# Kernel optimization log

Measured on AMD Instinct MI355X. Metric: run time of the kernel, lower is better.

## Reference

```python
import jax, jax.numpy as jnp
import numpy as np

EMBED_DIM = 1024
NUM_HEADS = 16
HEAD_DIM = EMBED_DIM // NUM_HEADS


def setup_inputs() -> dict:
    key = jax.random.key(0)
    ks = jax.random.split(key, 9)
    s = 1.0 / np.sqrt(EMBED_DIM)
    mk = lambda k: jax.random.uniform(k, (EMBED_DIM, EMBED_DIM), jnp.float32, -s, s)
    bk = lambda k: jax.random.uniform(k, (EMBED_DIM,), jnp.float32, -s, s)
    return {
        "input_tensor": jax.random.normal(ks[0], (4, 2048, EMBED_DIM), jnp.float32),
        "wq": mk(ks[1]), "bq": bk(ks[2]),
        "wk": mk(ks[3]), "bk_": bk(ks[4]),
        "wv": mk(ks[5]), "bv": bk(ks[6]),
        "wo": mk(ks[7]), "bo": bk(ks[8]),
    }


def reference(input_tensor, wq, bq, wk, bk_, wv, bv, wo, bo):
    B, S, E = input_tensor.shape
    H, D = NUM_HEADS, HEAD_DIM
    # torch Linear: y = x @ W.T + b
    q = input_tensor @ wq.T + bq
    k = input_tensor @ wk.T + bk_
    v = input_tensor @ wv.T + bv
    q = q.reshape(B, S, H, D).transpose(0, 2, 1, 3)  # [B,H,S,D]
    k = k.reshape(B, S, H, D).transpose(0, 2, 1, 3)
    v = v.reshape(B, S, H, D).transpose(0, 2, 1, 3)
    scores = jnp.einsum('bhsd,bhtd->bhst', q, k) / jnp.sqrt(jnp.float32(D))
    attn = jax.nn.softmax(scores, axis=-1)  # dropout p=0 -> identity
    out = jnp.einsum('bhst,bhtd->bhsd', attn, v)
    out = out.transpose(0, 2, 1, 3).reshape(B, S, E)
    return out @ wo.T + bo
```

## Files before the change

### kernel.cpp

```cpp
#include <hip/hip_runtime.h>

typedef __bf16 bf16x8 __attribute__((ext_vector_type(8)));
typedef float  f32x4  __attribute__((ext_vector_type(4)));
typedef float  f32x16 __attribute__((ext_vector_type(16)));
typedef unsigned u32x4 __attribute__((ext_vector_type(4)));

#define NB 4
#define SEQ 2048
#define EMB 1024
#define NH 16
#define HD 64
#define MTOT (NB * SEQ)

__device__ __forceinline__ unsigned short f2bf(float f) {
    unsigned u = __float_as_uint(f);
    return (unsigned short)((u + 0x7fffu + ((u >> 16) & 1u)) >> 16);
}

__device__ __forceinline__ void gload16(const void* g, void* l) {
    __builtin_amdgcn_global_load_lds(
        (const __attribute__((address_space(1))) unsigned int*)g,
        (__attribute__((address_space(3))) unsigned int*)l,
        16, 0, 0);
}

__global__ __launch_bounds__(256) void cast_f32_bf16(
    const float* __restrict__ src, unsigned short* __restrict__ dst, int n4) {
    int i = blockIdx.x * 256 + threadIdx.x;
    if (i < n4) {
        float4 v = ((const float4*)src)[i];
        ushort4 r;
        r.x = f2bf(v.x); r.y = f2bf(v.y); r.z = f2bf(v.z); r.w = f2bf(v.w);
        ((ushort4*)dst)[i] = r;
    }
}

__global__ __launch_bounds__(256) void cast4_f32_bf16(
    const float* __restrict__ a, const float* __restrict__ b,
    const float* __restrict__ c, const float* __restrict__ d,
    unsigned short* __restrict__ oa, unsigned short* __restrict__ ob,
    unsigned short* __restrict__ oc, unsigned short* __restrict__ od) {
    int which = blockIdx.x >> 10;
    int i = (blockIdx.x & 1023) * 256 + threadIdx.x;
    const float* src = which == 0 ? a : which == 1 ? b : which == 2 ? c : d;
    unsigned short* dst = which == 0 ? oa : which == 1 ? ob : which == 2 ? oc : od;
    float4 v = ((const float4*)src)[i];
    ushort4 r;
    r.x = f2bf(v.x); r.y = f2bf(v.y); r.z = f2bf(v.z); r.w = f2bf(v.w);
    ((ushort4*)dst)[i] = r;
}

__global__ __launch_bounds__(256) void gemm_qkv(
    const unsigned short* __restrict__ A, const unsigned short* __restrict__ W3,
    const float* __restrict__ bq, const float* __restrict__ bk,
    const float* __restrict__ bv, unsigned short* __restrict__ Qo,
    unsigned short* __restrict__ Ko, unsigned short* __restrict__ Vto) {
    constexpr int K = EMB;
    __shared__ __align__(16) unsigned short As[128 * 64];
    __shared__ __align__(16) unsigned short Bs[128 * 64];

    const int lane = threadIdx.x & 63;
    const int wv   = threadIdx.x >> 6;
    const int wr   = wv >> 1, wc = wv & 1;
    const int m0   = blockIdx.y * 128, n0 = blockIdx.x * 128;
    const int proj = n0 >> 10;
    const float* bp = proj == 0 ? bq : proj == 1 ? bk : bv;
    const float oscale = proj == 0 ? 0.18033688011112043f : 1.0f;

    f32x4 acc[4][4];
#pragma unroll
    for (int a = 0; a < 4; ++a)
#pragma unroll
        for (int b = 0; b < 4; ++b) acc[a][b] = (f32x4){0.f, 0.f, 0.f, 0.f};

    const int gsw = ((lane & 7) ^ (lane >> 3)) * 8;
    for (int kt = 0; kt < K / 64; ++kt) {
        if (kt) __syncthreads();
#pragma unroll
        for (int j = 0; j < 4; ++j) {
            int rb = (wv * 4 + j) * 8;
            int r  = rb + (lane >> 3);
            gload16(A + (size_t)(m0 + r) * K + kt * 64 + gsw, &As[rb * 64]);
            gload16(W3 + (size_t)(n0 + r) * K + kt * 64 + gsw, &Bs[rb * 64]);
        }
        __syncthreads();
#pragma unroll
        for (int ks = 0; ks < 2; ++ks) {
            const int slot = ((ks * 4 + (lane >> 4)) ^ (lane & 7)) * 8;
            bf16x8 af[4], bf_[4];
#pragma unroll
            for (int x = 0; x < 4; ++x) {
                af[x]  = *(const bf16x8*)&As[(wr * 64 + x * 16 + (lane & 15)) * 64 + slot];
                bf_[x] = *(const bf16x8*)&Bs[(wc * 64 + x * 16 + (lane & 15)) * 64 + slot];
            }
#pragma unroll
            for (int mi = 0; mi < 4; ++mi)
#pragma unroll
                for (int ni = 0; ni < 4; ++ni)
                    acc[mi][ni] = __builtin_amdgcn_mfma_f32_16x16x32_bf16(
                        af[mi], bf_[ni], acc[mi][ni], 0, 0, 0);
        }
    }

#pragma unroll
    for (int mi = 0; mi < 4; ++mi) {
#pragma unroll
        for (int ni = 0; ni < 4; ++ni) {
            int n    = n0 + wc * 64 + ni * 16 + (lane & 15);
            int nloc = n & 1023;
            float bvv = bp[nloc];
            int h = nloc >> 6, d = nloc & 63;
#pragma unroll
            for (int i = 0; i < 4; ++i) {
                int m = m0 + wr * 64 + mi * 16 + (lane >> 4) * 4 + i;
                float v = (acc[mi][ni][i] + bvv) * oscale;
                int b = m >> 11, s = m & (SEQ - 1);
                if (proj == 0)
                    Qo[(((size_t)(b * NH + h) * SEQ + s) << 6) + d] = f2bf(v);
                else if (proj == 1)
                    Ko[(((size_t)(b * NH + h) * SEQ + s) << 6) + d] = f2bf(v);
                else
                    Vto[((size_t)(b * NH + h) * 64 + d) * SEQ + s] = f2bf(v);
            }
        }
    }
}

__global__ __launch_bounds__(256) void gemm_out(
    const unsigned short* __restrict__ A, const unsigned short* __restrict__ W,
    const float* __restrict__ bias, float* __restrict__ out) {
    constexpr int K = EMB;
    __shared__ __align__(16) unsigned short As[128 * 64];
    __shared__ __align__(16) unsigned short Bs[128 * 64];

    const int lane = threadIdx.x & 63;
    const int wv   = threadIdx.x >> 6;
    const int wr   = wv >> 1, wc = wv & 1;
    const int m0   = blockIdx.y * 128, n0 = blockIdx.x * 128;

    f32x4 acc[4][4];
#pragma unroll
    for (int a = 0; a < 4; ++a)
#pragma unroll
        for (int b = 0; b < 4; ++b) acc[a][b] = (f32x4){0.f, 0.f, 0.f, 0.f};

    const int gsw = ((lane & 7) ^ (lane >> 3)) * 8;
    for (int kt = 0; kt < K / 64; ++kt) {
        if (kt) __syncthreads();
#pragma unroll
        for (int j = 0; j < 4; ++j) {
            int rb = (wv * 4 + j) * 8;
            int r  = rb + (lane >> 3);
            gload16(A + (size_t)(m0 + r) * K + kt * 64 + gsw, &As[rb * 64]);
            gload16(W + (size_t)(n0 + r) * K + kt * 64 + gsw, &Bs[rb * 64]);
        }
        __syncthreads();
#pragma unroll
        for (int ks = 0; ks < 2; ++ks) {
            const int slot = ((ks * 4 + (lane >> 4)) ^ (lane & 7)) * 8;
            bf16x8 af[4], bf_[4];
#pragma unroll
            for (int x = 0; x < 4; ++x) {
                af[x]  = *(const bf16x8*)&As[(wr * 64 + x * 16 + (lane & 15)) * 64 + slot];
                bf_[x] = *(const bf16x8*)&Bs[(wc * 64 + x * 16 + (lane & 15)) * 64 + slot];
            }
#pragma unroll
            for (int mi = 0; mi < 4; ++mi)
#pragma unroll
                for (int ni = 0; ni < 4; ++ni)
                    acc[mi][ni] = __builtin_amdgcn_mfma_f32_16x16x32_bf16(
                        af[mi], bf_[ni], acc[mi][ni], 0, 0, 0);
        }
    }

#pragma unroll
    for (int mi = 0; mi < 4; ++mi) {
#pragma unroll
        for (int ni = 0; ni < 4; ++ni) {
            int n = n0 + wc * 64 + ni * 16 + (lane & 15);
            float bv = bias[n];
#pragma unroll
            for (int i = 0; i < 4; ++i) {
                int m = m0 + wr * 64 + mi * 16 + (lane >> 4) * 4 + i;
                out[(size_t)m * EMB + n] = acc[mi][ni][i] + bv;
            }
        }
    }
}

__global__ __launch_bounds__(512, 4) void attn_fwd(
    const unsigned short* __restrict__ Q, const unsigned short* __restrict__ K,
    const unsigned short* __restrict__ Vt, unsigned short* __restrict__ AO) {
    const int qt = blockIdx.x;
    const int bh = blockIdx.y;
    const int lane = threadIdx.x & 63;
    const int wv   = threadIdx.x >> 6;
    const int l31  = lane & 31;
    const int lh   = lane >> 5;

    __shared__ __align__(16) unsigned short Ks[2][64 * 64];
    __shared__ __align__(16) unsigned short Vs[2][64 * 64];

    const unsigned short* Kb = K + (size_t)bh * SEQ * HD;
    const unsigned short* Vb = Vt + (size_t)bh * HD * SEQ;

    const unsigned short* Qp = Q + ((size_t)bh * SEQ + qt * 256 + wv * 32 + l31) * HD + lh * 8;
    bf16x8 qfr[4];
#pragma unroll
    for (int kc = 0; kc < 4; ++kc) qfr[kc] = *(const bf16x8*)(Qp + kc * 16);

    f32x16 oT[2];
#pragma unroll
    for (int r = 0; r < 16; ++r) { oT[0][r] = 0.f; oT[1][r] = 0.f; }
    float lacc = 0.f;

    auto stageKV = [&](int buf, int t) {
        int r  = wv * 8 + (lane >> 3);
        int gs = (lane & 7) ^ (r & 7);
        gload16(Kb + (size_t)(t * 64 + r) * 64 + gs * 8, &Ks[buf][wv * 8 * 64]);
        gload16(Vb + (size_t)r * SEQ + t * 64 + gs * 8, &Vs[buf][wv * 8 * 64]);
    };

    stageKV(0, 0);

    for (int t = 0; t < SEQ / 64; ++t) {
        const int cur = t & 1;
        __syncthreads();
        if (t + 1 < SEQ / 64) stageKV(cur ^ 1, t + 1);

#pragma unroll
        for (int sub = 0; sub < 2; ++sub) {
            f32x16 st;
#pragma unroll
            for (int r = 0; r < 16; ++r) st[r] = 0.f;
            const int krow = sub * 32 + l31;
            __builtin_amdgcn_s_setprio(1);
#pragma unroll
            for (int kc = 0; kc < 4; ++kc) {
                int slot = (kc * 2 + lh) ^ (krow & 7);
                bf16x8 kf = *(const bf16x8*)&Ks[cur][krow * 64 + slot * 8];
                st = __builtin_amdgcn_mfma_f32_32x32x16_bf16(kf, qfr[kc], st, 0, 0, 0);
            }
            __builtin_amdgcn_s_setprio(0);

            unsigned w0, w1, w2, w3, w4, w5, w6, w7;
#define EXPPK(WI, RA, RB)                                                     \
            {                                                                 \
                float pa = __builtin_amdgcn_exp2f(st[RA]);                    \
                float pb = __builtin_amdgcn_exp2f(st[RB]);                    \
                lacc += pa + pb;                                              \
                asm("v_cvt_pk_bf16_f32 %0, %1, %2" : "=v"(WI) : "v"(pa), "v"(pb)); \
            }
            EXPPK(w0, 0, 1)  EXPPK(w1, 2, 3)  EXPPK(w2, 4, 5)  EXPPK(w3, 6, 7)
            EXPPK(w4, 8, 9)  EXPPK(w5, 10, 11) EXPPK(w6, 12, 13) EXPPK(w7, 14, 15)
#undef EXPPK
            asm volatile("v_permlane32_swap_b32 %0, %1" : "+v"(w0), "+v"(w2));
            asm volatile("v_permlane32_swap_b32 %0, %1" : "+v"(w1), "+v"(w3));
            asm volatile("v_permlane32_swap_b32 %0, %1" : "+v"(w4), "+v"(w6));
            asm volatile("v_permlane32_swap_b32 %0, %1" : "+v"(w5), "+v"(w7));
            u32x4 a0 = {w0, w1, w2, w3};
            u32x4 a1 = {w4, w5, w6, w7};
            bf16x8 pf0 = __builtin_bit_cast(bf16x8, a0);
            bf16x8 pf1 = __builtin_bit_cast(bf16x8, a1);

            __builtin_amdgcn_s_setprio(1);
#pragma unroll
            for (int dt = 0; dt < 2; ++dt) {
                int d = dt * 32 + l31;
#pragma unroll
                for (int ks = 0; ks < 2; ++ks) {
                    int slot = (sub * 4 + ks * 2 + lh) ^ (d & 7);
                    bf16x8 vf = *(const bf16x8*)&Vs[cur][d * 64 + slot * 8];
                    oT[dt] = __builtin_amdgcn_mfma_f32_32x32x16_bf16(
                        vf, ks ? pf1 : pf0, oT[dt], 0, 0, 0);
                }
            }
            __builtin_amdgcn_s_setprio(0);
        }
    }

    float l = lacc + __shfl_xor(lacc, 32);
    float inv = 1.0f / l;
    const int b = bh >> 4, h = bh & 15;
    const int q = qt * 256 + wv * 32 + l31;
    unsigned short* aor = AO + (((size_t)b * SEQ + q) * NH + h) * HD;
#pragma unroll
    for (int dt = 0; dt < 2; ++dt) {
#pragma unroll
        for (int g = 0; g < 4; ++g) {
            ushort4 o;
            o.x = f2bf(oT[dt][g * 4 + 0] * inv);
            o.y = f2bf(oT[dt][g * 4 + 1] * inv);
            o.z = f2bf(oT[dt][g * 4 + 2] * inv);
            o.w = f2bf(oT[dt][g * 4 + 3] * inv);
            *(ushort4*)(aor + dt * 32 + g * 8 + lh * 4) = o;
        }
    }
}

extern "C" void kernel_launch(void* const* d_in, const int* in_sizes, int n_in,
                              void* d_out, int out_size, void* d_ws, size_t ws_size,
                              hipStream_t stream) {
    const float* X  = (const float*)d_in[0];
    const float* wq = (const float*)d_in[1];
    const float* bq = (const float*)d_in[2];
    const float* wk = (const float*)d_in[3];
    const float* bk = (const float*)d_in[4];
    const float* wv = (const float*)d_in[5];
    const float* bv = (const float*)d_in[6];
    const float* wo = (const float*)d_in[7];
    const float* bo = (const float*)d_in[8];
    float* out = (float*)d_out;

    unsigned short* ws = (unsigned short*)d_ws;
    const size_t XE = (size_t)MTOT * EMB;
    const size_t WE = (size_t)EMB * EMB;
    unsigned short* Xb  = ws;
    unsigned short* Wqb = ws + XE;
    unsigned short* Wkb = Wqb + WE;
    unsigned short* Wvb = Wkb + WE;
    unsigned short* Wob = Wvb + WE;
    unsigned short* Qb  = Wob + WE;
    unsigned short* Kb  = Qb + XE;
    unsigned short* Vtb = Kb + XE;
    unsigned short* AOb = Xb;

    cast_f32_bf16<<<(int)(XE / 4 / 256), 256, 0, stream>>>(X, Xb, (int)(XE / 4));
    cast4_f32_bf16<<<4096, 256, 0, stream>>>(wq, wk, wv, wo, Wqb, Wkb, Wvb, Wob);

    gemm_qkv<<<dim3(3 * EMB / 128, MTOT / 128), 256, 0, stream>>>(
        Xb, Wqb, bq, bk, bv, Qb, Kb, Vtb);

    attn_fwd<<<dim3(SEQ / 256, NB * NH), 512, 0, stream>>>(Qb, Kb, Vtb, AOb);

    gemm_out<<<dim3(EMB / 128, MTOT / 128), 256, 0, stream>>>(AOb, Wob, bo, out);
}
```

Before: 189.9 us.

## Process two 32-row query groups per wave to reuse K/V fragments in attention

Each wave in the attention kernel now owns 64 query rows split into two 32-row groups. The K fragments loaded from LDS are reused for both score MFMAs, and the V fragments for both PV MFMAs, halving LDS reads per unit of MFMA work. Blocks shrink to 4 waves, each wave staging two rows of K/V, and the grid becomes 1D with bh as the fast index so blocks sharing a head's K/V run close together. Register pressure roughly doubles for accumulators and Q fragments, and the launch bounds change to 256 threads with 2 blocks per SIMD, which may lower occupancy.

```diff
diff --git a/kernel.cpp b/kernel.cpp
--- a/kernel.cpp
+++ b/kernel.cpp
@@ -188,11 +188,11 @@
     }
 }
 
-__global__ __launch_bounds__(512, 4) void attn_fwd(
+__global__ __launch_bounds__(256, 2) void attn_fwd(
     const unsigned short* __restrict__ Q, const unsigned short* __restrict__ K,
     const unsigned short* __restrict__ Vt, unsigned short* __restrict__ AO) {
-    const int qt = blockIdx.x;
-    const int bh = blockIdx.y;
+    const int qt = blockIdx.x >> 6;
+    const int bh = blockIdx.x & 63;
     const int lane = threadIdx.x & 63;
     const int wv   = threadIdx.x >> 6;
     const int l31  = lane & 31;
@@ -204,21 +204,33 @@
     const unsigned short* Kb = K + (size_t)bh * SEQ * HD;
     const unsigned short* Vb = Vt + (size_t)bh * HD * SEQ;
 
-    const unsigned short* Qp = Q + ((size_t)bh * SEQ + qt * 256 + wv * 32 + l31) * HD + lh * 8;
-    bf16x8 qfr[4];
-#pragma unroll
-    for (int kc = 0; kc < 4; ++kc) qfr[kc] = *(const bf16x8*)(Qp + kc * 16);
-
-    f32x16 oT[2];
-#pragma unroll
-    for (int r = 0; r < 16; ++r) { oT[0][r] = 0.f; oT[1][r] = 0.f; }
-    float lacc = 0.f;
+    bf16x8 qfr[2][4];
+#pragma unroll
+    for (int qg = 0; qg < 2; ++qg) {
+        const unsigned short* Qp =
+            Q + ((size_t)bh * SEQ + qt * 256 + wv * 64 + qg * 32 + l31) * HD + lh * 8;
+#pragma unroll
+        for (int kc = 0; kc < 4; ++kc) qfr[qg][kc] = *(const bf16x8*)(Qp + kc * 16);
+    }
+
+    f32x16 oT[2][2];
+#pragma unroll
+    for (int qg = 0; qg < 2; ++qg)
+#pragma unroll
+        for (int dt = 0; dt < 2; ++dt)
+#pragma unroll
+            for (int r = 0; r < 16; ++r) oT[qg][dt][r] = 0.f;
+    float lacc[2] = {0.f, 0.f};
 
     auto stageKV = [&](int buf, int t) {
-        int r  = wv * 8 + (lane >> 3);
-        int gs = (lane & 7) ^ (r & 7);
-        gload16(Kb + (size_t)(t * 64 + r) * 64 + gs * 8, &Ks[buf][wv * 8 * 64]);
-        gload16(Vb + (size_t)r * SEQ + t * 64 + gs * 8, &Vs[buf][wv * 8 * 64]);
+#pragma unroll
+        for (int j = 0; j < 2; ++j) {
+            int rb = wv * 16 + j * 8;
+            int r  = rb + (lane >> 3);
+            int gs = (lane & 7) ^ (r & 7);
+            gload16(Kb + (size_t)(t * 64 + r) * 64 + gs * 8, &Ks[buf][rb * 64]);
+            gload16(Vb + (size_t)r * SEQ + t * 64 + gs * 8, &Vs[buf][rb * 64]);
+        }
     };
 
     stageKV(0, 0);
@@ -230,38 +242,52 @@
 
 #pragma unroll
         for (int sub = 0; sub < 2; ++sub) {
-            f32x16 st;
-#pragma unroll
-            for (int r = 0; r < 16; ++r) st[r] = 0.f;
             const int krow = sub * 32 + l31;
-            __builtin_amdgcn_s_setprio(1);
+            bf16x8 kf[4];
 #pragma unroll
             for (int kc = 0; kc < 4; ++kc) {
                 int slot = (kc * 2 + lh) ^ (krow & 7);
-                bf16x8 kf = *(const bf16x8*)&Ks[cur][krow * 64 + slot * 8];
-                st = __builtin_amdgcn_mfma_f32_32x32x16_bf16(kf, qfr[kc], st, 0, 0, 0);
-            }
+                kf[kc] = *(const bf16x8*)&Ks[cur][krow * 64 + slot * 8];
+            }
+            f32x16 stA, stB;
+#pragma unroll
+            for (int r = 0; r < 16; ++r) { stA[r] = 0.f; stB[r] = 0.f; }
+            __builtin_amdgcn_s_setprio(1);
+#pragma unroll
+            for (int kc = 0; kc < 4; ++kc)
+                stA = __builtin_amdgcn_mfma_f32_32x32x16_bf16(kf[kc], qfr[0][kc], stA, 0, 0, 0);
+#pragma unroll
+            for (int kc = 0; kc < 4; ++kc)
+                stB = __builtin_amdgcn_mfma_f32_32x32x16_bf16(kf[kc], qfr[1][kc], stB, 0, 0, 0);
             __builtin_amdgcn_s_setprio(0);
 
-            unsigned w0, w1, w2, w3, w4, w5, w6, w7;
-#define EXPPK(WI, RA, RB)                                                     \
-            {                                                                 \
-                float pa = __builtin_amdgcn_exp2f(st[RA]);                    \
-                float pb = __builtin_amdgcn_exp2f(st[RB]);                    \
-                lacc += pa + pb;                                              \
-                asm("v_cvt_pk_bf16_f32 %0, %1, %2" : "=v"(WI) : "v"(pa), "v"(pb)); \
-            }
-            EXPPK(w0, 0, 1)  EXPPK(w1, 2, 3)  EXPPK(w2, 4, 5)  EXPPK(w3, 6, 7)
-            EXPPK(w4, 8, 9)  EXPPK(w5, 10, 11) EXPPK(w6, 12, 13) EXPPK(w7, 14, 15)
-#undef EXPPK
-            asm volatile("v_permlane32_swap_b32 %0, %1" : "+v"(w0), "+v"(w2));
-            asm volatile("v_permlane32_swap_b32 %0, %1" : "+v"(w1), "+v"(w3));
-            asm volatile("v_permlane32_swap_b32 %0, %1" : "+v"(w4), "+v"(w6));
-            asm volatile("v_permlane32_swap_b32 %0, %1" : "+v"(w5), "+v"(w7));
-            u32x4 a0 = {w0, w1, w2, w3};
-            u32x4 a1 = {w4, w5, w6, w7};
-            bf16x8 pf0 = __builtin_bit_cast(bf16x8, a0);
-            bf16x8 pf1 = __builtin_bit_cast(bf16x8, a1);
+            bf16x8 pfA0, pfA1, pfB0, pfB1;
+#define SOFTMAX(ST, PF0, PF1, LACC)                                              \
+            {                                                                    \
+                unsigned w0, w1, w2, w3, w4, w5, w6, w7;                         \
+                float pa, pb;                                                    \
+_Pragma("clang diagnostic push")                                                 \
+                pa = __builtin_amdgcn_exp2f(ST[0]);  pb = __builtin_amdgcn_exp2f(ST[1]);  LACC += pa + pb; asm("v_cvt_pk_bf16_f32 %0, %1, %2" : "=v"(w0) : "v"(pa), "v"(pb)); \
+                pa = __builtin_amdgcn_exp2f(ST[2]);  pb = __builtin_amdgcn_exp2f(ST[3]);  LACC += pa + pb; asm("v_cvt_pk_bf16_f32 %0, %1, %2" : "=v"(w1) : "v"(pa), "v"(pb)); \
+                pa = __builtin_amdgcn_exp2f(ST[4]);  pb = __builtin_amdgcn_exp2f(ST[5]);  LACC += pa + pb; asm("v_cvt_pk_bf16_f32 %0, %1, %2" : "=v"(w2) : "v"(pa), "v"(pb)); \
+                pa = __builtin_amdgcn_exp2f(ST[6]);  pb = __builtin_amdgcn_exp2f(ST[7]);  LACC += pa + pb; asm("v_cvt_pk_bf16_f32 %0, %1, %2" : "=v"(w3) : "v"(pa), "v"(pb)); \
+                pa = __builtin_amdgcn_exp2f(ST[8]);  pb = __builtin_amdgcn_exp2f(ST[9]);  LACC += pa + pb; asm("v_cvt_pk_bf16_f32 %0, %1, %2" : "=v"(w4) : "v"(pa), "v"(pb)); \
+                pa = __builtin_amdgcn_exp2f(ST[10]); pb = __builtin_amdgcn_exp2f(ST[11]); LACC += pa + pb; asm("v_cvt_pk_bf16_f32 %0, %1, %2" : "=v"(w5) : "v"(pa), "v"(pb)); \
+                pa = __builtin_amdgcn_exp2f(ST[12]); pb = __builtin_amdgcn_exp2f(ST[13]); LACC += pa + pb; asm("v_cvt_pk_bf16_f32 %0, %1, %2" : "=v"(w6) : "v"(pa), "v"(pb)); \
+                pa = __builtin_amdgcn_exp2f(ST[14]); pb = __builtin_amdgcn_exp2f(ST[15]); LACC += pa + pb; asm("v_cvt_pk_bf16_f32 %0, %1, %2" : "=v"(w7) : "v"(pa), "v"(pb)); \
+_Pragma("clang diagnostic pop")                                                  \
+                asm volatile("v_permlane32_swap_b32 %0, %1" : "+v"(w0), "+v"(w2)); \
+                asm volatile("v_permlane32_swap_b32 %0, %1" : "+v"(w1), "+v"(w3)); \
+                asm volatile("v_permlane32_swap_b32 %0, %1" : "+v"(w4), "+v"(w6)); \
+                asm volatile("v_permlane32_swap_b32 %0, %1" : "+v"(w5), "+v"(w7)); \
+                u32x4 a0 = {w0, w1, w2, w3};                                     \
+                u32x4 a1 = {w4, w5, w6, w7};                                     \
+                PF0 = __builtin_bit_cast(bf16x8, a0);                            \
+                PF1 = __builtin_bit_cast(bf16x8, a1);                            \
+            }
+            SOFTMAX(stA, pfA0, pfA1, lacc[0])
+            SOFTMAX(stB, pfB0, pfB1, lacc[1])
+#undef SOFTMAX
 
             __builtin_amdgcn_s_setprio(1);
 #pragma unroll
@@ -271,29 +297,34 @@
                 for (int ks = 0; ks < 2; ++ks) {
                     int slot = (sub * 4 + ks * 2 + lh) ^ (d & 7);
                     bf16x8 vf = *(const bf16x8*)&Vs[cur][d * 64 + slot * 8];
-                    oT[dt] = __builtin_amdgcn_mfma_f32_32x32x16_bf16(
-                        vf, ks ? pf1 : pf0, oT[dt], 0, 0, 0);
+                    oT[0][dt] = __builtin_amdgcn_mfma_f32_32x32x16_bf16(
+                        vf, ks ? pfA1 : pfA0, oT[0][dt], 0, 0, 0);
+                    oT[1][dt] = __builtin_amdgcn_mfma_f32_32x32x16_bf16(
+                        vf, ks ? pfB1 : pfB0, oT[1][dt], 0, 0, 0);
                 }
             }
             __builtin_amdgcn_s_setprio(0);
         }
     }
 
-    float l = lacc + __shfl_xor(lacc, 32);
-    float inv = 1.0f / l;
     const int b = bh >> 4, h = bh & 15;
-    const int q = qt * 256 + wv * 32 + l31;
-    unsigned short* aor = AO + (((size_t)b * SEQ + q) * NH + h) * HD;
-#pragma unroll
-    for (int dt = 0; dt < 2; ++dt) {
-#pragma unroll
-        for (int g = 0; g < 4; ++g) {
-            ushort4 o;
-            o.x = f2bf(oT[dt][g * 4 + 0] * inv);
-            o.y = f2bf(oT[dt][g * 4 + 1] * inv);
-            o.z = f2bf(oT[dt][g * 4 + 2] * inv);
-            o.w = f2bf(oT[dt][g * 4 + 3] * inv);
-            *(ushort4*)(aor + dt * 32 + g * 8 + lh * 4) = o;
+#pragma unroll
+    for (int qg = 0; qg < 2; ++qg) {
+        float l = lacc[qg] + __shfl_xor(lacc[qg], 32);
+        float inv = 1.0f / l;
+        const int q = qt * 256 + wv * 64 + qg * 32 + l31;
+        unsigned short* aor = AO + (((size_t)b * SEQ + q) * NH + h) * HD;
+#pragma unroll
+        for (int dt = 0; dt < 2; ++dt) {
+#pragma unroll
+            for (int g = 0; g < 4; ++g) {
+                ushort4 o;
+                o.x = f2bf(oT[qg][dt][g * 4 + 0] * inv);
+                o.y = f2bf(oT[qg][dt][g * 4 + 1] * inv);
+                o.z = f2bf(oT[qg][dt][g * 4 + 2] * inv);
+                o.w = f2bf(oT[qg][dt][g * 4 + 3] * inv);
+                *(ushort4*)(aor + dt * 32 + g * 8 + lh * 4) = o;
+            }
         }
     }
 }
@@ -331,7 +362,7 @@
     gemm_qkv<<<dim3(3 * EMB / 128, MTOT / 128), 256, 0, stream>>>(
         Xb, Wqb, bq, bk, bv, Qb, Kb, Vtb);
 
-    attn_fwd<<<dim3(SEQ / 256, NB * NH), 512, 0, stream>>>(Qb, Kb, Vtb, AOb);
+    attn_fwd<<<512, 256, 0, stream>>>(Qb, Kb, Vtb, AOb);
 
     gemm_out<<<dim3(EMB / 128, MTOT / 128), 256, 0, stream>>>(AOb, Wob, bo, out);
 }
```

Result: no change. 190.9 us (+0.5%).
